# Optimization experiments

Hardware: AMD Instinct MI355X
Metric: run time of the kernel (lower is better)

## Reference

```python
import jax, jax.numpy as jnp
import numpy as np


def setup_inputs() -> dict:
    key = jax.random.key(0)
    k1, k2 = jax.random.split(key)
    L, O, N, D = 512, 512, 64, 512
    x = jax.random.normal(k1, (L, N, D), dtype=jnp.float32)
    upfold = jax.random.normal(k2, (O, N, D), dtype=jnp.float32)
    return {"x": x, "upfold": upfold}


def reference(x, upfold):
    # x: [L, N, D], upfold: [O, N, D]
    D = x.shape[-1]
    scale = 1.0 / jnp.sqrt(jnp.asarray(D, dtype=x.dtype))
    # affinities: [L, O, N]
    affinities = jnp.einsum('lnd,ond->lon', x, upfold) * scale
    # sigmoid-attention (no softmax normalization), centered at 0
    weights = jax.nn.sigmoid(affinities) - 0.5
    # features: [L, N, D]
    features = jnp.einsum('lon,ond->lnd', weights, upfold)
    return features
```

## Files before the change

### kernel.cpp

```cpp
#include <hip/hip_runtime.h>
#include <hip/hip_bf16.h>
#include <stdint.h>


typedef __attribute__((ext_vector_type(8))) short short8;
typedef __attribute__((ext_vector_type(4))) float f32x4;

__device__ __forceinline__ uint16_t f2bf(float f) {
    uint32_t u = __builtin_bit_cast(uint32_t, f);
    uint32_t r = u + 0x7FFFu + ((u >> 16) & 1u);
    return (uint16_t)(r >> 16);
}
__device__ __forceinline__ uint32_t cvt2(float a, float b) {
    return (uint32_t)f2bf(a) | ((uint32_t)f2bf(b) << 16);
}

__global__ __launch_bounds__(256) void kPrepUp(const float* __restrict__ up,
                                               uint16_t* __restrict__ ub,
                                               uint16_t* __restrict__ ut) {
    __shared__ float tile[64][65];
    int wgid = blockIdx.x;
    int iq = wgid >> 3;
    int n  = (wgid & 7) * 8 + (iq >> 6);
    int r  = iq & 63;
    int o0 = (r >> 3) << 6, d0 = (r & 7) << 6;
    int tid = threadIdx.x;
    int i  = tid >> 2;
    int jq = (tid & 3) << 4;

    const float* src = up + ((size_t)(o0 + i) * 64 + n) * 512 + d0 + jq;
    float v[16];
    #pragma unroll
    for (int c = 0; c < 16; c += 4) {
        float4 q = *reinterpret_cast<const float4*>(src + c);
        v[c] = q.x; v[c+1] = q.y; v[c+2] = q.z; v[c+3] = q.w;
        tile[i][jq+c] = q.x; tile[i][jq+c+1] = q.y;
        tile[i][jq+c+2] = q.z; tile[i][jq+c+3] = q.w;
    }
    uint32_t pk[8];
    if (ub) {
        #pragma unroll
        for (int c = 0; c < 8; ++c) pk[c] = cvt2(v[2*c], v[2*c+1]);
        uint16_t* udst = ub + ((size_t)n * 512 + o0 + i) * 512 + d0 + jq;
        *reinterpret_cast<uint4*>(udst)     = *reinterpret_cast<const uint4*>(pk);
        *reinterpret_cast<uint4*>(udst + 8) = *reinterpret_cast<const uint4*>(pk + 4);
    }
    __syncthreads();
    #pragma unroll
    for (int c = 0; c < 8; ++c) pk[c] = cvt2(tile[jq + 2*c][i], tile[jq + 2*c + 1][i]);
    uint16_t* tdst = ut + ((size_t)n * 512 + d0 + i) * 512 + o0 + jq;
    *reinterpret_cast<uint4*>(tdst)     = *reinterpret_cast<const uint4*>(pk);
    *reinterpret_cast<uint4*>(tdst + 8) = *reinterpret_cast<const uint4*>(pk + 4);
}

__global__ __launch_bounds__(256) void kPrepX(const float* __restrict__ x,
                                              uint16_t* __restrict__ xb) {
    int b = blockIdx.x;
    int tid = threadIdx.x;
    int row = b * 4 + (tid >> 6);
    int l = row >> 6, n = row & 63;
    int d0 = (tid & 63) * 8;
    const float* src = x + (size_t)row * 512 + d0;
    float4 v0 = *reinterpret_cast<const float4*>(src);
    float4 v1 = *reinterpret_cast<const float4*>(src + 4);
    uint32_t pk[4] = {cvt2(v0.x, v0.y), cvt2(v0.z, v0.w),
                      cvt2(v1.x, v1.y), cvt2(v1.z, v1.w)};
    *reinterpret_cast<uint4*>(xb + ((size_t)n * 512 + l) * 512 + d0) =
        *reinterpret_cast<const uint4*>(pk);
}

template<int MODE>
__global__ __launch_bounds__(512) void kGemmP(const uint16_t* __restrict__ A,
                                              const uint16_t* __restrict__ B,
                                              void* __restrict__ outp) {
    __shared__ __align__(16) uint16_t As[4][8192];
    __shared__ __align__(16) uint16_t Bs[4][8192];
    int bid = blockIdx.x;
    int n  = (bid & 7) * 8 + (bid >> 5);
    int t  = (bid >> 3) & 3;
    int l0 = (t >> 1) << 8, c0 = (t & 1) << 8;
    int tid = threadIdx.x, lane = tid & 63, wid = tid >> 6;
    int wr = wid >> 2, wc = wid & 3;

    const char* An = (const char*)(A + (size_t)n * 262144);
    const char* Bn = (const char*)(B + (size_t)n * 262144);

    int s1 = tid, s2 = tid + 512;
    int r1 = s1 >> 2, r2 = s2 >> 2;
    int cg1 = (s1 & 3) ^ ((r1 >> 1) & 3);
    int cg2 = (s2 & 3) ^ ((r2 >> 1) & 3);
    const char* gA1 = An + (size_t)(l0 + r1) * 1024 + cg1 * 16;
    const char* gA2 = An + (size_t)(l0 + r2) * 1024 + cg2 * 16;
    const char* gB1 = Bn + (size_t)(c0 + r1) * 1024 + cg1 * 16;
    const char* gB2 = Bn + (size_t)(c0 + r2) * 1024 + cg2 * 16;

    f32x4 acc[8][4];
    #pragma unroll
    for (int m = 0; m < 8; ++m)
        #pragma unroll
        for (int nf = 0; nf < 4; ++nf) acc[m][nf] = (f32x4)(0.f);

    auto STAGE = [&](int buf, int kt) {
        int ko = kt * 64;
        uint16_t* lA = &As[buf][wid * 512];
        uint16_t* lB = &Bs[buf][wid * 512];
        __builtin_amdgcn_global_load_lds(
            (const __attribute__((address_space(1))) uint32_t*)(gA1 + ko),
            (__attribute__((address_space(3))) uint32_t*)(lA), 16, 0, 0);
        __builtin_amdgcn_global_load_lds(
            (const __attribute__((address_space(1))) uint32_t*)(gA2 + ko),
            (__attribute__((address_space(3))) uint32_t*)(lA + 4096), 16, 0, 0);
        __builtin_amdgcn_global_load_lds(
            (const __attribute__((address_space(1))) uint32_t*)(gB1 + ko),
            (__attribute__((address_space(3))) uint32_t*)(lB), 16, 0, 0);
        __builtin_amdgcn_global_load_lds(
            (const __attribute__((address_space(1))) uint32_t*)(gB2 + ko),
            (__attribute__((address_space(3))) uint32_t*)(lB + 4096), 16, 0, 0);
    };

    STAGE(0, 0);
    STAGE(1, 1);
    STAGE(2, 2);
    asm volatile("s_waitcnt vmcnt(8)" ::: "memory");
    __builtin_amdgcn_s_barrier();
    __builtin_amdgcn_sched_barrier(0);

    int g = lane >> 4;
    #pragma unroll
    for (int kt = 0; kt < 16; ++kt) {
        const int cur = kt & 3;
        if (kt < 13) STAGE((kt + 3) & 3, kt + 3);
        const char* Ac = (const char*)As[cur];
        const char* Bc = (const char*)Bs[cur];
        short8 a[8], bb[4];
        #pragma unroll
        for (int nf = 0; nf < 4; ++nf) {
            int row = wc * 64 + nf * 16 + (lane & 15);
            int off = row * 64 + ((g ^ ((row >> 1) & 3)) << 4);
            bb[nf] = *reinterpret_cast<const short8*>(Bc + off);
        }
        #pragma unroll
        for (int m = 0; m < 8; ++m) {
            int row = wr * 128 + m * 16 + (lane & 15);
            int off = row * 64 + ((g ^ ((row >> 1) & 3)) << 4);
            a[m] = *reinterpret_cast<const short8*>(Ac + off);
        }
        __builtin_amdgcn_s_setprio(1);
        #pragma unroll
        for (int m = 0; m < 8; ++m)
            #pragma unroll
            for (int nf = 0; nf < 4; ++nf)
                acc[m][nf] = __builtin_amdgcn_mfma_f32_16x16x32_bf16(
                    a[m], bb[nf], acc[m][nf], 0, 0, 0);
        __builtin_amdgcn_s_setprio(0);
        if (kt < 13) {
            asm volatile("s_waitcnt vmcnt(8)" ::: "memory");
            __builtin_amdgcn_s_barrier();
            __builtin_amdgcn_sched_barrier(0);
        } else if (kt == 13) {
            asm volatile("s_waitcnt vmcnt(4)" ::: "memory");
            __builtin_amdgcn_s_barrier();
            __builtin_amdgcn_sched_barrier(0);
        } else if (kt == 14) {
            asm volatile("s_waitcnt vmcnt(0)" ::: "memory");
            __builtin_amdgcn_s_barrier();
            __builtin_amdgcn_sched_barrier(0);
        }
    }

    if constexpr (MODE == 1) {
        uint16_t* Wn = (uint16_t*)outp + (size_t)n * 262144;
        const float scale = 0.044194173824159216f;
        #pragma unroll
        for (int m = 0; m < 8; ++m) {
            int lrow0 = l0 + wr * 128 + m * 16 + ((lane >> 4) << 2);
            #pragma unroll
            for (int nf = 0; nf < 4; ++nf) {
                int ocol = c0 + wc * 64 + nf * 16 + (lane & 15);
                #pragma unroll
                for (int r = 0; r < 4; ++r) {
                    float aff = acc[m][nf][r] * scale;
                    float w = 1.f / (1.f + __expf(-aff)) - 0.5f;
                    Wn[(size_t)(lrow0 + r) * 512 + ocol] = f2bf(w);
                }
            }
        }
    } else {
        float* On = (float*)outp;
        #pragma unroll
        for (int m = 0; m < 8; ++m) {
            int lrow0 = l0 + wr * 128 + m * 16 + ((lane >> 4) << 2);
            #pragma unroll
            for (int nf = 0; nf < 4; ++nf) {
                int dcol = c0 + wc * 64 + nf * 16 + (lane & 15);
                #pragma unroll
                for (int r = 0; r < 4; ++r)
                    On[((size_t)(lrow0 + r) * 64 + n) * 512 + dcol] = acc[m][nf][r];
            }
        }
    }
}

__global__ __launch_bounds__(256) void kGemm1f32(const float* __restrict__ x,
                                                 const float* __restrict__ up,
                                                 uint16_t* __restrict__ W) {
    __shared__ uint16_t As[128 * 64];
    __shared__ uint16_t Bs[128 * 64];
    int b   = blockIdx.x;
    int n   = b >> 4;
    int t   = b & 15;
    int l0  = (t >> 2) << 7, o0 = (t & 3) << 7;
    int tid = threadIdx.x, lane = tid & 63, wid = tid >> 6;
    int wr = wid >> 1, wc = wid & 1;

    f32x4 acc[4][4];
    #pragma unroll
    for (int m = 0; m < 4; ++m)
        #pragma unroll
        for (int nf = 0; nf < 4; ++nf) acc[m][nf] = (f32x4)(0.f);

    int srow = tid >> 1;
    int kh   = (tid & 1) * 32;
    int swz  = (srow & 7) << 4;
    const float* aSrc = x  + ((size_t)(l0 + srow) * 64 + n) * 512 + kh;
    const float* bSrc = up + ((size_t)(o0 + srow) * 64 + n) * 512 + kh;

    for (int kt = 0; kt < 8; ++kt) {
        __syncthreads();
        const float* pA = aSrc + kt * 64;
        const float* pB = bSrc + kt * 64;
        #pragma unroll
        for (int c2 = 0; c2 < 4; ++c2) {
            float4 a0 = *reinterpret_cast<const float4*>(pA + c2 * 8);
            float4 a1 = *reinterpret_cast<const float4*>(pA + c2 * 8 + 4);
            float4 b0 = *reinterpret_cast<const float4*>(pB + c2 * 8);
            float4 b1 = *reinterpret_cast<const float4*>(pB + c2 * 8 + 4);
            uint32_t pa[4] = {cvt2(a0.x,a0.y), cvt2(a0.z,a0.w), cvt2(a1.x,a1.y), cvt2(a1.z,a1.w)};
            uint32_t pb[4] = {cvt2(b0.x,b0.y), cvt2(b0.z,b0.w), cvt2(b1.x,b1.y), cvt2(b1.z,b1.w)};
            int off = srow * 128 + (((kh * 2) + c2 * 16) ^ swz);
            *reinterpret_cast<uint4*>((char*)As + off) = *reinterpret_cast<const uint4*>(pa);
            *reinterpret_cast<uint4*>((char*)Bs + off) = *reinterpret_cast<const uint4*>(pb);
        }
        __syncthreads();
        #pragma unroll
        for (int kk = 0; kk < 2; ++kk) {
            short8 a[4], bf[4];
            int kbyte = kk * 64 + ((lane >> 4) * 16);
            #pragma unroll
            for (int m = 0; m < 4; ++m) {
                int row = wr * 64 + m * 16 + (lane & 15);
                int off = row * 128 + (kbyte ^ ((row & 7) << 4));
                a[m] = *reinterpret_cast<const short8*>((char*)As + off);
            }
            #pragma unroll
            for (int nf = 0; nf < 4; ++nf) {
                int row = wc * 64 + nf * 16 + (lane & 15);
                int off = row * 128 + (kbyte ^ ((row & 7) << 4));
                bf[nf] = *reinterpret_cast<const short8*>((char*)Bs + off);
            }
            #pragma unroll
            for (int m = 0; m < 4; ++m)
                #pragma unroll
                for (int nf = 0; nf < 4; ++nf)
                    acc[m][nf] = __builtin_amdgcn_mfma_f32_16x16x32_bf16(
                        a[m], bf[nf], acc[m][nf], 0, 0, 0);
        }
    }
    const float scale = 0.044194173824159216f;
    #pragma unroll
    for (int m = 0; m < 4; ++m) {
        int lrow0 = l0 + wr * 64 + m * 16 + ((lane >> 4) << 2);
        #pragma unroll
        for (int nf = 0; nf < 4; ++nf) {
            int ocol = o0 + wc * 64 + nf * 16 + (lane & 15);
            #pragma unroll
            for (int r = 0; r < 4; ++r) {
                float aff = acc[m][nf][r] * scale;
                float w = 1.f / (1.f + __expf(-aff)) - 0.5f;
                W[((size_t)n * 512 + (lrow0 + r)) * 512 + ocol] = f2bf(w);
            }
        }
    }
}

__global__ __launch_bounds__(256) void kGemm2Mid(const uint16_t* __restrict__ W,
                                                 const uint16_t* __restrict__ ut,
                                                 float* __restrict__ out) {
    __shared__ uint16_t As[8192];
    __shared__ uint16_t Bs[8192];
    int d = blockIdx.x;
    int n  = (d & 7) * 8 + (d >> 7);
    int t  = (d >> 3) & 15;
    int l0 = (t >> 2) << 7, c0 = (t & 3) << 7;
    int tid = threadIdx.x, lane = tid & 63, wid = tid >> 6;
    int wr = wid >> 1, wc = wid & 1;

    const char* An = (const char*)(W  + (size_t)n * 262144);
    const char* Bn = (const char*)(ut + (size_t)n * 262144);
    int rsub  = lane >> 3;
    int sbyte = ((lane & 7) ^ rsub) << 4;
    const char* gA = An + (size_t)(l0 + wid * 32 + rsub) * 1024 + sbyte;
    const char* gB = Bn + (size_t)(c0 + wid * 32 + rsub) * 1024 + sbyte;
    uint16_t* lA = As + wid * 2048;
    uint16_t* lB = Bs + wid * 2048;

    f32x4 acc[4][4];
    #pragma unroll
    for (int m = 0; m < 4; ++m)
        #pragma unroll
        for (int nf = 0; nf < 4; ++nf) acc[m][nf] = (f32x4)(0.f);

    for (int kt = 0; kt < 8; ++kt) {
        if (kt) __syncthreads();
        #pragma unroll
        for (int j = 0; j < 4; ++j) {
            __builtin_amdgcn_global_load_lds(
                (const __attribute__((address_space(1))) uint32_t*)(gA + kt * 128 + j * 8192),
                (__attribute__((address_space(3))) uint32_t*)(lA + j * 512), 16, 0, 0);
            __builtin_amdgcn_global_load_lds(
                (const __attribute__((address_space(1))) uint32_t*)(gB + kt * 128 + j * 8192),
                (__attribute__((address_space(3))) uint32_t*)(lB + j * 512), 16, 0, 0);
        }
        __syncthreads();
        #pragma unroll
        for (int kk = 0; kk < 2; ++kk) {
            short8 a[4], bb[4];
            int kbyte = kk * 64 + ((lane >> 4) * 16);
            #pragma unroll
            for (int m = 0; m < 4; ++m) {
                int row = wr * 64 + m * 16 + (lane & 15);
                int off = row * 128 + (kbyte ^ ((row & 7) << 4));
                a[m] = *reinterpret_cast<const short8*>((const char*)As + off);
            }
            #pragma unroll
            for (int nf = 0; nf < 4; ++nf) {
                int row = wc * 64 + nf * 16 + (lane & 15);
                int off = row * 128 + (kbyte ^ ((row & 7) << 4));
                bb[nf] = *reinterpret_cast<const short8*>((const char*)Bs + off);
            }
            #pragma unroll
            for (int m = 0; m < 4; ++m)
                #pragma unroll
                for (int nf = 0; nf < 4; ++nf)
                    acc[m][nf] = __builtin_amdgcn_mfma_f32_16x16x32_bf16(
                        a[m], bb[nf], acc[m][nf], 0, 0, 0);
        }
    }
    #pragma unroll
    for (int m = 0; m < 4; ++m) {
        int lrow0 = l0 + wr * 64 + m * 16 + ((lane >> 4) << 2);
        #pragma unroll
        for (int nf = 0; nf < 4; ++nf) {
            int dcol = c0 + wc * 64 + nf * 16 + (lane & 15);
            #pragma unroll
            for (int r = 0; r < 4; ++r)
                out[((size_t)(lrow0 + r) * 64 + n) * 512 + dcol] = acc[m][nf][r];
        }
    }
}

__global__ __launch_bounds__(256) void kNaive(const float* __restrict__ x,
                                              const float* __restrict__ up,
                                              float* __restrict__ out) {
    __shared__ float xr[512];
    __shared__ float w[512];
    int b = blockIdx.x;
    int l = b >> 6, n = b & 63;
    int tid = threadIdx.x;
    const float* xrow = x + ((size_t)l * 64 + n) * 512;
    xr[tid] = xrow[tid];
    xr[tid + 256] = xrow[tid + 256];
    __syncthreads();
    const float scale = 0.044194173824159216f;
    #pragma unroll
    for (int oo = 0; oo < 2; ++oo) {
        int o = tid + oo * 256;
        const float* ur = up + ((size_t)o * 64 + n) * 512;
        float s = 0.f;
        for (int dd = 0; dd < 512; ++dd) s += xr[dd] * ur[dd];
        w[o] = 1.f / (1.f + __expf(-s * scale)) - 0.5f;
    }
    __syncthreads();
    #pragma unroll
    for (int dd = 0; dd < 2; ++dd) {
        int d = tid + dd * 256;
        float f = 0.f;
        for (int o = 0; o < 512; ++o)
            f += w[o] * up[((size_t)o * 64 + n) * 512 + d];
        out[((size_t)l * 64 + n) * 512 + d] = f;
    }
}

extern "C" void kernel_launch(void* const* d_in, const int* in_sizes, int n_in,
                              void* d_out, int out_size, void* d_ws, size_t ws_size,
                              hipStream_t stream) {
    const float* x  = (const float*)d_in[0];
    const float* up = (const float*)d_in[1];
    float* out = (float*)d_out;

    const size_t MB32 = (size_t)64 * 512 * 512 * 2;
    if (ws_size >= 4 * MB32) {
        uint16_t* XB = (uint16_t*)d_ws;
        uint16_t* UB = XB + 16777216;
        uint16_t* UT = UB + 16777216;
        uint16_t* W  = UT + 16777216;
        kPrepUp<<<4096, 256, 0, stream>>>(up, UB, UT);
        kPrepX <<<8192, 256, 0, stream>>>(x, XB);
        kGemmP<1><<<256, 512, 0, stream>>>(XB, UB, W);
        kGemmP<2><<<256, 512, 0, stream>>>(W, UT, out);
    } else if (ws_size >= 2 * MB32) {
        uint16_t* UT = (uint16_t*)d_ws;
        uint16_t* W  = UT + 16777216;
        kPrepUp<<<4096, 256, 0, stream>>>(up, nullptr, UT);
        kGemm1f32<<<1024, 256, 0, stream>>>(x, up, W);
        kGemm2Mid<<<1024, 256, 0, stream>>>(W, UT, out);
    } else {
        kNaive<<<512 * 64, 256, 0, stream>>>(x, up, out);
    }
}
```

Measured before the change: 110.3 us.

## Fuse x bf16 conversion into first GEMM and split upfold prep into convert+transpose

Removes the separate x-to-bf16 prep kernel by having the first GEMM load fp32 x rows into registers, convert them with packed bf16 instructions, and write them swizzled into LDS. The loads are software-pipelined alongside async global-to-LDS loads of B. Upfold prep is split into a plain convert kernel and a bf16 LDS transpose kernel that reads the converted copy, so the transpose moves half the bytes. The change drops one 32 MB intermediate and its round trip and lowers the workspace requirement, at the cost of extra register pressure and more complex waitcnt scheduling in the GEMM.

After: 110.9 us. Within noise of the previous version (+0.5%).

```diff
diff --git a/kernel.cpp b/kernel.cpp
--- a/kernel.cpp
+++ b/kernel.cpp
@@ -14,59 +14,206 @@
 __device__ __forceinline__ uint32_t cvt2(float a, float b) {
     return (uint32_t)f2bf(a) | ((uint32_t)f2bf(b) << 16);
 }
-
-__global__ __launch_bounds__(256) void kPrepUp(const float* __restrict__ up,
-                                               uint16_t* __restrict__ ub,
-                                               uint16_t* __restrict__ ut) {
-    __shared__ float tile[64][65];
-    int wgid = blockIdx.x;
-    int iq = wgid >> 3;
-    int n  = (wgid & 7) * 8 + (iq >> 6);
-    int r  = iq & 63;
-    int o0 = (r >> 3) << 6, d0 = (r & 7) << 6;
-    int tid = threadIdx.x;
-    int i  = tid >> 2;
-    int jq = (tid & 3) << 4;
-
-    const float* src = up + ((size_t)(o0 + i) * 64 + n) * 512 + d0 + jq;
-    float v[16];
-    #pragma unroll
-    for (int c = 0; c < 16; c += 4) {
-        float4 q = *reinterpret_cast<const float4*>(src + c);
-        v[c] = q.x; v[c+1] = q.y; v[c+2] = q.z; v[c+3] = q.w;
-        tile[i][jq+c] = q.x; tile[i][jq+c+1] = q.y;
-        tile[i][jq+c+2] = q.z; tile[i][jq+c+3] = q.w;
-    }
-    uint32_t pk[8];
-    if (ub) {
-        #pragma unroll
-        for (int c = 0; c < 8; ++c) pk[c] = cvt2(v[2*c], v[2*c+1]);
-        uint16_t* udst = ub + ((size_t)n * 512 + o0 + i) * 512 + d0 + jq;
-        *reinterpret_cast<uint4*>(udst)     = *reinterpret_cast<const uint4*>(pk);
-        *reinterpret_cast<uint4*>(udst + 8) = *reinterpret_cast<const uint4*>(pk + 4);
-    }
-    __syncthreads();
-    #pragma unroll
-    for (int c = 0; c < 8; ++c) pk[c] = cvt2(tile[jq + 2*c][i], tile[jq + 2*c + 1][i]);
-    uint16_t* tdst = ut + ((size_t)n * 512 + d0 + i) * 512 + o0 + jq;
-    *reinterpret_cast<uint4*>(tdst)     = *reinterpret_cast<const uint4*>(pk);
-    *reinterpret_cast<uint4*>(tdst + 8) = *reinterpret_cast<const uint4*>(pk + 4);
-}
-
-__global__ __launch_bounds__(256) void kPrepX(const float* __restrict__ x,
-                                              uint16_t* __restrict__ xb) {
-    int b = blockIdx.x;
-    int tid = threadIdx.x;
-    int row = b * 4 + (tid >> 6);
-    int l = row >> 6, n = row & 63;
-    int d0 = (tid & 63) * 8;
-    const float* src = x + (size_t)row * 512 + d0;
+__device__ __forceinline__ uint32_t pkbf(float lo, float hi) {
+    uint32_t r;
+    asm("v_cvt_pk_bf16_f32 %0, %1, %2" : "=v"(r) : "v"(lo), "v"(hi));
+    return r;
+}
+
+__global__ __launch_bounds__(256) void kPrepU(const float* __restrict__ up,
+                                              uint16_t* __restrict__ ub) {
+    int blk  = blockIdx.x;
+    int rest = blk >> 3;
+    int n    = (blk & 7) * 8 + (rest >> 7);
+    int o    = (rest & 127) * 4 + (threadIdx.x >> 6);
+    int d0   = (threadIdx.x & 63) * 8;
+    const float* src = up + ((size_t)o * 64 + n) * 512 + d0;
     float4 v0 = *reinterpret_cast<const float4*>(src);
     float4 v1 = *reinterpret_cast<const float4*>(src + 4);
     uint32_t pk[4] = {cvt2(v0.x, v0.y), cvt2(v0.z, v0.w),
                       cvt2(v1.x, v1.y), cvt2(v1.z, v1.w)};
-    *reinterpret_cast<uint4*>(xb + ((size_t)n * 512 + l) * 512 + d0) =
+    *reinterpret_cast<uint4*>(ub + ((size_t)n * 512 + o) * 512 + d0) =
         *reinterpret_cast<const uint4*>(pk);
+}
+
+__global__ __launch_bounds__(256) void kPrepT(const uint16_t* __restrict__ ub,
+                                              uint16_t* __restrict__ ut) {
+    __shared__ uint32_t tl[512 * 20];
+    int blk  = blockIdx.x;
+    int rest = blk >> 3;
+    int n    = (blk & 7) * 8 + (rest >> 4);
+    int d0   = (rest & 15) * 32;
+    int tid  = threadIdx.x;
+
+    #pragma unroll
+    for (int e = 0; e < 2; ++e) {
+        int o = tid * 2 + e;
+        const uint16_t* src = ub + ((size_t)n * 512 + o) * 512 + d0;
+        uint4 q0 = reinterpret_cast<const uint4*>(src)[0];
+        uint4 q1 = reinterpret_cast<const uint4*>(src)[1];
+        uint4 q2 = reinterpret_cast<const uint4*>(src)[2];
+        uint4 q3 = reinterpret_cast<const uint4*>(src)[3];
+        int sw = ((o >> 6) & 3) << 2;
+        uint32_t* row = tl + o * 20;
+        *reinterpret_cast<uint4*>(row + (0  ^ sw)) = q0;
+        *reinterpret_cast<uint4*>(row + (4  ^ sw)) = q1;
+        *reinterpret_cast<uint4*>(row + (8  ^ sw)) = q2;
+        *reinterpret_cast<uint4*>(row + (12 ^ sw)) = q3;
+    }
+    __syncthreads();
+
+    int d   = tid >> 3;
+    int seg = (tid & 7) * 64;
+    int c   = d >> 1;
+    int sh  = (d & 1) * 16;
+    uint32_t ow[32];
+    #pragma unroll
+    for (int j = 0; j < 32; ++j) {
+        int o0 = seg + 2 * j;
+        int sw = ((o0 >> 6) & 3) << 2;
+        uint32_t w0 = tl[o0 * 20 + (c ^ sw)];
+        uint32_t w1 = tl[(o0 + 1) * 20 + (c ^ sw)];
+        ow[j] = ((w0 >> sh) & 0xFFFFu) | (((w1 >> sh) & 0xFFFFu) << 16);
+    }
+    uint16_t* dst = ut + ((size_t)n * 512 + d0 + d) * 512 + seg;
+    #pragma unroll
+    for (int q = 0; q < 8; ++q)
+        reinterpret_cast<uint4*>(dst)[q] = *reinterpret_cast<const uint4*>(ow + q * 4);
+}
+
+__global__ __launch_bounds__(512, 1) void kGemmP1x(const float* __restrict__ x,
+                                                   const uint16_t* __restrict__ ub,
+                                                   uint16_t* __restrict__ W) {
+    __shared__ __align__(16) uint16_t As[4][8192];
+    __shared__ __align__(16) uint16_t Bs[4][8192];
+    int bid = blockIdx.x;
+    int n  = (bid & 7) * 8 + (bid >> 5);
+    int t  = (bid >> 3) & 3;
+    int l0 = (t >> 1) << 8, c0 = (t & 1) << 8;
+    int tid = threadIdx.x, lane = tid & 63, wid = tid >> 6;
+    int wr = wid >> 2, wc = wid & 3;
+
+    const char* Bn = (const char*)(ub + (size_t)n * 262144);
+    int s1 = tid, s2 = tid + 512;
+    int r1b = s1 >> 2, r2b = s2 >> 2;
+    int cg1 = (s1 & 3) ^ ((r1b >> 1) & 3);
+    int cg2 = (s2 & 3) ^ ((r2b >> 1) & 3);
+    const char* gB1 = Bn + (size_t)(c0 + r1b) * 1024 + cg1 * 16;
+    const char* gB2 = Bn + (size_t)(c0 + r2b) * 1024 + cg2 * 16;
+
+    int ra  = tid >> 1;
+    int h   = tid & 1;
+    int swA = (ra >> 1) & 3;
+    const float* xA = x + ((size_t)(l0 + ra) * 64 + n) * 512 + h * 16;
+    int offA0 = ra * 64 + (((2 * h)     ^ swA) << 4);
+    int offA1 = ra * 64 + (((2 * h + 1) ^ swA) << 4);
+
+    f32x4 acc[8][4];
+    #pragma unroll
+    for (int m = 0; m < 8; ++m)
+        #pragma unroll
+        for (int nf = 0; nf < 4; ++nf) acc[m][nf] = (f32x4)(0.f);
+
+    auto STAGEB = [&](int buf, int kt) {
+        int ko = kt * 64;
+        uint16_t* lB = &Bs[buf][wid * 512];
+        __builtin_amdgcn_global_load_lds(
+            (const __attribute__((address_space(1))) uint32_t*)(gB1 + ko),
+            (__attribute__((address_space(3))) uint32_t*)(lB), 16, 0, 0);
+        __builtin_amdgcn_global_load_lds(
+            (const __attribute__((address_space(1))) uint32_t*)(gB2 + ko),
+            (__attribute__((address_space(3))) uint32_t*)(lB + 4096), 16, 0, 0);
+    };
+    float4 rg[2][4];
+    auto LOADR = [&](int set, int kt) {
+        const float* p = xA + kt * 32;
+        #pragma unroll
+        for (int j = 0; j < 4; ++j)
+            rg[set][j] = *reinterpret_cast<const float4*>(p + j * 4);
+    };
+    auto CVTW = [&](int set, int abuf) {
+        uint32_t pk[8];
+        #pragma unroll
+        for (int j = 0; j < 4; ++j) {
+            pk[2*j]   = pkbf(rg[set][j].x, rg[set][j].y);
+            pk[2*j+1] = pkbf(rg[set][j].z, rg[set][j].w);
+        }
+        char* base = (char*)As[abuf];
+        *reinterpret_cast<uint4*>(base + offA0) = *reinterpret_cast<const uint4*>(pk);
+        *reinterpret_cast<uint4*>(base + offA1) = *reinterpret_cast<const uint4*>(pk + 4);
+    };
+
+    LOADR(0, 0); CVTW(0, 0);
+    LOADR(0, 1); CVTW(0, 1);
+    LOADR(0, 2);
+    STAGEB(0, 0); STAGEB(1, 1); STAGEB(2, 2);
+    asm volatile("s_waitcnt vmcnt(4) lgkmcnt(0)" ::: "memory");
+    __builtin_amdgcn_s_barrier();
+    __builtin_amdgcn_sched_barrier(0);
+
+    int g = lane >> 4;
+    #pragma unroll
+    for (int kt = 0; kt < 16; ++kt) {
+        const int cur = kt & 3;
+        if (kt < 13) {
+            LOADR((kt + 1) & 1, kt + 3);
+            STAGEB((kt + 3) & 3, kt + 3);
+        }
+        const char* Ac = (const char*)As[cur];
+        const char* Bc = (const char*)Bs[cur];
+        short8 a[8], bb[4];
+        #pragma unroll
+        for (int nf = 0; nf < 4; ++nf) {
+            int row = wc * 64 + nf * 16 + (lane & 15);
+            int off = row * 64 + ((g ^ ((row >> 1) & 3)) << 4);
+            bb[nf] = *reinterpret_cast<const short8*>(Bc + off);
+        }
+        #pragma unroll
+        for (int m = 0; m < 8; ++m) {
+            int row = wr * 128 + m * 16 + (lane & 15);
+            int off = row * 64 + ((g ^ ((row >> 1) & 3)) << 4);
+            a[m] = *reinterpret_cast<const short8*>(Ac + off);
+        }
+        __builtin_amdgcn_s_setprio(1);
+        #pragma unroll
+        for (int m = 0; m < 8; ++m)
+            #pragma unroll
+            for (int nf = 0; nf < 4; ++nf)
+                acc[m][nf] = __builtin_amdgcn_mfma_f32_16x16x32_bf16(
+                    a[m], bb[nf], acc[m][nf], 0, 0, 0);
+        __builtin_amdgcn_s_setprio(0);
+        if (kt < 14) CVTW(kt & 1, (kt + 2) & 3);
+        if (kt < 13) {
+            asm volatile("s_waitcnt vmcnt(8) lgkmcnt(0)" ::: "memory");
+            __builtin_amdgcn_s_barrier();
+            __builtin_amdgcn_sched_barrier(0);
+        } else if (kt == 13) {
+            asm volatile("s_waitcnt vmcnt(2) lgkmcnt(0)" ::: "memory");
+            __builtin_amdgcn_s_barrier();
+            __builtin_amdgcn_sched_barrier(0);
+        } else if (kt == 14) {
+            asm volatile("s_waitcnt vmcnt(0) lgkmcnt(0)" ::: "memory");
+            __builtin_amdgcn_s_barrier();
+            __builtin_amdgcn_sched_barrier(0);
+        }
+    }
+
+    uint16_t* Wn = W + (size_t)n * 262144;
+    const float scale = 0.044194173824159216f;
+    #pragma unroll
+    for (int m = 0; m < 8; ++m) {
+        int lrow0 = l0 + wr * 128 + m * 16 + ((lane >> 4) << 2);
+        #pragma unroll
+        for (int nf = 0; nf < 4; ++nf) {
+            int ocol = c0 + wc * 64 + nf * 16 + (lane & 15);
+            #pragma unroll
+            for (int r = 0; r < 4; ++r) {
+                float aff = acc[m][nf][r] * scale;
+                float w = 1.f / (1.f + __expf(-aff)) - 0.5f;
+                Wn[(size_t)(lrow0 + r) * 512 + ocol] = f2bf(w);
+            }
+        }
+    }
 }
 
 template<int MODE>
@@ -84,7 +231,6 @@
 
     const char* An = (const char*)(A + (size_t)n * 262144);
     const char* Bn = (const char*)(B + (size_t)n * 262144);
-
     int s1 = tid, s2 = tid + 512;
     int r1 = s1 >> 2, r2 = s2 >> 2;
     int cg1 = (s1 & 3) ^ ((r1 >> 1) & 3);
@@ -201,6 +347,44 @@
     }
 }
 
+__global__ __launch_bounds__(256) void kPrepUp(const float* __restrict__ up,
+                                               uint16_t* __restrict__ ub,
+                                               uint16_t* __restrict__ ut) {
+    __shared__ float tile[64][65];
+    int wgid = blockIdx.x;
+    int iq = wgid >> 3;
+    int n  = (wgid & 7) * 8 + (iq >> 6);
+    int r  = iq & 63;
+    int o0 = (r >> 3) << 6, d0 = (r & 7) << 6;
+    int tid = threadIdx.x;
+    int i  = tid >> 2;
+    int jq = (tid & 3) << 4;
+
+    const float* src = up + ((size_t)(o0 + i) * 64 + n) * 512 + d0 + jq;
+    float v[16];
+    #pragma unroll
+    for (int c = 0; c < 16; c += 4) {
+        float4 q = *reinterpret_cast<const float4*>(src + c);
+        v[c] = q.x; v[c+1] = q.y; v[c+2] = q.z; v[c+3] = q.w;
+        tile[i][jq+c] = q.x; tile[i][jq+c+1] = q.y;
+        tile[i][jq+c+2] = q.z; tile[i][jq+c+3] = q.w;
+    }
+    uint32_t pk[8];
+    if (ub) {
+        #pragma unroll
+        for (int c = 0; c < 8; ++c) pk[c] = cvt2(v[2*c], v[2*c+1]);
+        uint16_t* udst = ub + ((size_t)n * 512 + o0 + i) * 512 + d0 + jq;
+        *reinterpret_cast<uint4*>(udst)     = *reinterpret_cast<const uint4*>(pk);
+        *reinterpret_cast<uint4*>(udst + 8) = *reinterpret_cast<const uint4*>(pk + 4);
+    }
+    __syncthreads();
+    #pragma unroll
+    for (int c = 0; c < 8; ++c) pk[c] = cvt2(tile[jq + 2*c][i], tile[jq + 2*c + 1][i]);
+    uint16_t* tdst = ut + ((size_t)n * 512 + d0 + i) * 512 + o0 + jq;
+    *reinterpret_cast<uint4*>(tdst)     = *reinterpret_cast<const uint4*>(pk);
+    *reinterpret_cast<uint4*>(tdst + 8) = *reinterpret_cast<const uint4*>(pk + 4);
+}
+
 __global__ __launch_bounds__(256) void kGemm1f32(const float* __restrict__ x,
                                                  const float* __restrict__ up,
                                                  uint16_t* __restrict__ W) {
@@ -399,14 +583,13 @@
     float* out = (float*)d_out;
 
     const size_t MB32 = (size_t)64 * 512 * 512 * 2;
-    if (ws_size >= 4 * MB32) {
-        uint16_t* XB = (uint16_t*)d_ws;
-        uint16_t* UB = XB + 16777216;
+    if (ws_size >= 3 * MB32) {
+        uint16_t* UB = (uint16_t*)d_ws;
         uint16_t* UT = UB + 16777216;
         uint16_t* W  = UT + 16777216;
-        kPrepUp<<<4096, 256, 0, stream>>>(up, UB, UT);
-        kPrepX <<<8192, 256, 0, stream>>>(x, XB);
-        kGemmP<1><<<256, 512, 0, stream>>>(XB, UB, W);
+        kPrepU<<<8192, 256, 0, stream>>>(up, UB);
+        kPrepT<<<1024, 256, 0, stream>>>(UB, UT);
+        kGemmP1x<<<256, 512, 0, stream>>>(x, UB, W);
         kGemmP<2><<<256, 512, 0, stream>>>(W, UT, out);
     } else if (ws_size >= 2 * MB32) {
         uint16_t* UT = (uint16_t*)d_ws;
```

## Split upfold prep into row-wise bf16 cast and separate bf16 transpose kernel

Applied to the files above, without the earlier changes.

Replaces the combined fp32 tile-transpose prep with a simple coalesced fp32-to-bf16 cast kernel, followed by a new kernel that transposes the already-converted bf16 buffer through a swizzled LDS tile. The aim is fully coalesced row-wise fp32 reads and a transpose that moves half as many bytes. The cost is an extra launch and re-reading the bf16 copy of upfold. The s_setprio hints around the MFMA loop in the GEMM are also removed.

Result: slower. 117.9 us (+6.9%).

```diff
diff --git a/kernel.cpp b/kernel.cpp
--- a/kernel.cpp
+++ b/kernel.cpp
@@ -15,42 +15,20 @@
     return (uint32_t)f2bf(a) | ((uint32_t)f2bf(b) << 16);
 }
 
-__global__ __launch_bounds__(256) void kPrepUp(const float* __restrict__ up,
-                                               uint16_t* __restrict__ ub,
-                                               uint16_t* __restrict__ ut) {
-    __shared__ float tile[64][65];
-    int wgid = blockIdx.x;
-    int iq = wgid >> 3;
-    int n  = (wgid & 7) * 8 + (iq >> 6);
-    int r  = iq & 63;
-    int o0 = (r >> 3) << 6, d0 = (r & 7) << 6;
-    int tid = threadIdx.x;
-    int i  = tid >> 2;
-    int jq = (tid & 3) << 4;
-
-    const float* src = up + ((size_t)(o0 + i) * 64 + n) * 512 + d0 + jq;
-    float v[16];
-    #pragma unroll
-    for (int c = 0; c < 16; c += 4) {
-        float4 q = *reinterpret_cast<const float4*>(src + c);
-        v[c] = q.x; v[c+1] = q.y; v[c+2] = q.z; v[c+3] = q.w;
-        tile[i][jq+c] = q.x; tile[i][jq+c+1] = q.y;
-        tile[i][jq+c+2] = q.z; tile[i][jq+c+3] = q.w;
-    }
-    uint32_t pk[8];
-    if (ub) {
-        #pragma unroll
-        for (int c = 0; c < 8; ++c) pk[c] = cvt2(v[2*c], v[2*c+1]);
-        uint16_t* udst = ub + ((size_t)n * 512 + o0 + i) * 512 + d0 + jq;
-        *reinterpret_cast<uint4*>(udst)     = *reinterpret_cast<const uint4*>(pk);
-        *reinterpret_cast<uint4*>(udst + 8) = *reinterpret_cast<const uint4*>(pk + 4);
-    }
-    __syncthreads();
-    #pragma unroll
-    for (int c = 0; c < 8; ++c) pk[c] = cvt2(tile[jq + 2*c][i], tile[jq + 2*c + 1][i]);
-    uint16_t* tdst = ut + ((size_t)n * 512 + d0 + i) * 512 + o0 + jq;
-    *reinterpret_cast<uint4*>(tdst)     = *reinterpret_cast<const uint4*>(pk);
-    *reinterpret_cast<uint4*>(tdst + 8) = *reinterpret_cast<const uint4*>(pk + 4);
+__global__ __launch_bounds__(256) void kPrepU(const float* __restrict__ up,
+                                              uint16_t* __restrict__ ub) {
+    int blk  = blockIdx.x;
+    int rest = blk >> 3;
+    int n    = (blk & 7) * 8 + (rest >> 7);
+    int o    = (rest & 127) * 4 + (threadIdx.x >> 6);
+    int d0   = (threadIdx.x & 63) * 8;
+    const float* src = up + ((size_t)o * 64 + n) * 512 + d0;
+    float4 v0 = *reinterpret_cast<const float4*>(src);
+    float4 v1 = *reinterpret_cast<const float4*>(src + 4);
+    uint32_t pk[4] = {cvt2(v0.x, v0.y), cvt2(v0.z, v0.w),
+                      cvt2(v1.x, v1.y), cvt2(v1.z, v1.w)};
+    *reinterpret_cast<uint4*>(ub + ((size_t)n * 512 + o) * 512 + d0) =
+        *reinterpret_cast<const uint4*>(pk);
 }
 
 __global__ __launch_bounds__(256) void kPrepX(const float* __restrict__ x,
@@ -67,6 +45,51 @@
                       cvt2(v1.x, v1.y), cvt2(v1.z, v1.w)};
     *reinterpret_cast<uint4*>(xb + ((size_t)n * 512 + l) * 512 + d0) =
         *reinterpret_cast<const uint4*>(pk);
+}
+
+__global__ __launch_bounds__(256) void kPrepT(const uint16_t* __restrict__ ub,
+                                              uint16_t* __restrict__ ut) {
+    __shared__ uint32_t tl[512 * 20];
+    int blk  = blockIdx.x;
+    int rest = blk >> 3;
+    int n    = (blk & 7) * 8 + (rest >> 4);
+    int d0   = (rest & 15) * 32;
+    int tid  = threadIdx.x;
+
+    #pragma unroll
+    for (int e = 0; e < 2; ++e) {
+        int o = tid * 2 + e;
+        const uint16_t* src = ub + ((size_t)n * 512 + o) * 512 + d0;
+        uint4 q0 = reinterpret_cast<const uint4*>(src)[0];
+        uint4 q1 = reinterpret_cast<const uint4*>(src)[1];
+        uint4 q2 = reinterpret_cast<const uint4*>(src)[2];
+        uint4 q3 = reinterpret_cast<const uint4*>(src)[3];
+        int sw = ((o >> 6) & 3) << 2;
+        uint32_t* row = tl + o * 20;
+        *reinterpret_cast<uint4*>(row + (0  ^ sw)) = q0;
+        *reinterpret_cast<uint4*>(row + (4  ^ sw)) = q1;
+        *reinterpret_cast<uint4*>(row + (8  ^ sw)) = q2;
+        *reinterpret_cast<uint4*>(row + (12 ^ sw)) = q3;
+    }
+    __syncthreads();
+
+    int d   = tid >> 3;
+    int seg = (tid & 7) * 64;
+    int c   = d >> 1;
+    int sh  = (d & 1) * 16;
+    uint32_t ow[32];
+    #pragma unroll
+    for (int j = 0; j < 32; ++j) {
+        int o0 = seg + 2 * j;
+        int sw = ((o0 >> 6) & 3) << 2;
+        uint32_t w0 = tl[o0 * 20 + (c ^ sw)];
+        uint32_t w1 = tl[(o0 + 1) * 20 + (c ^ sw)];
+        ow[j] = ((w0 >> sh) & 0xFFFFu) | (((w1 >> sh) & 0xFFFFu) << 16);
+    }
+    uint16_t* dst = ut + ((size_t)n * 512 + d0 + d) * 512 + seg;
+    #pragma unroll
+    for (int q = 0; q < 8; ++q)
+        reinterpret_cast<uint4*>(dst)[q] = *reinterpret_cast<const uint4*>(ow + q * 4);
 }
 
 template<int MODE>
@@ -145,14 +168,12 @@
             int off = row * 64 + ((g ^ ((row >> 1) & 3)) << 4);
             a[m] = *reinterpret_cast<const short8*>(Ac + off);
         }
-        __builtin_amdgcn_s_setprio(1);
         #pragma unroll
         for (int m = 0; m < 8; ++m)
             #pragma unroll
             for (int nf = 0; nf < 4; ++nf)
                 acc[m][nf] = __builtin_amdgcn_mfma_f32_16x16x32_bf16(
                     a[m], bb[nf], acc[m][nf], 0, 0, 0);
-        __builtin_amdgcn_s_setprio(0);
         if (kt < 13) {
             asm volatile("s_waitcnt vmcnt(8)" ::: "memory");
             __builtin_amdgcn_s_barrier();
@@ -199,6 +220,44 @@
             }
         }
     }
+}
+
+__global__ __launch_bounds__(256) void kPrepUp(const float* __restrict__ up,
+                                               uint16_t* __restrict__ ub,
+                                               uint16_t* __restrict__ ut) {
+    __shared__ float tile[64][65];
+    int wgid = blockIdx.x;
+    int iq = wgid >> 3;
+    int n  = (wgid & 7) * 8 + (iq >> 6);
+    int r  = iq & 63;
+    int o0 = (r >> 3) << 6, d0 = (r & 7) << 6;
+    int tid = threadIdx.x;
+    int i  = tid >> 2;
+    int jq = (tid & 3) << 4;
+
+    const float* src = up + ((size_t)(o0 + i) * 64 + n) * 512 + d0 + jq;
+    float v[16];
+    #pragma unroll
+    for (int c = 0; c < 16; c += 4) {
+        float4 q = *reinterpret_cast<const float4*>(src + c);
+        v[c] = q.x; v[c+1] = q.y; v[c+2] = q.z; v[c+3] = q.w;
+        tile[i][jq+c] = q.x; tile[i][jq+c+1] = q.y;
+        tile[i][jq+c+2] = q.z; tile[i][jq+c+3] = q.w;
+    }
+    uint32_t pk[8];
+    if (ub) {
+        #pragma unroll
+        for (int c = 0; c < 8; ++c) pk[c] = cvt2(v[2*c], v[2*c+1]);
+        uint16_t* udst = ub + ((size_t)n * 512 + o0 + i) * 512 + d0 + jq;
+        *reinterpret_cast<uint4*>(udst)     = *reinterpret_cast<const uint4*>(pk);
+        *reinterpret_cast<uint4*>(udst + 8) = *reinterpret_cast<const uint4*>(pk + 4);
+    }
+    __syncthreads();
+    #pragma unroll
+    for (int c = 0; c < 8; ++c) pk[c] = cvt2(tile[jq + 2*c][i], tile[jq + 2*c + 1][i]);
+    uint16_t* tdst = ut + ((size_t)n * 512 + d0 + i) * 512 + o0 + jq;
+    *reinterpret_cast<uint4*>(tdst)     = *reinterpret_cast<const uint4*>(pk);
+    *reinterpret_cast<uint4*>(tdst + 8) = *reinterpret_cast<const uint4*>(pk + 4);
 }
 
 __global__ __launch_bounds__(256) void kGemm1f32(const float* __restrict__ x,
@@ -404,8 +463,9 @@
         uint16_t* UB = XB + 16777216;
         uint16_t* UT = UB + 16777216;
         uint16_t* W  = UT + 16777216;
-        kPrepUp<<<4096, 256, 0, stream>>>(up, UB, UT);
-        kPrepX <<<8192, 256, 0, stream>>>(x, XB);
+        kPrepU<<<8192, 256, 0, stream>>>(up, UB);
+        kPrepX<<<8192, 256, 0, stream>>>(x, XB);
+        kPrepT<<<1024, 256, 0, stream>>>(UB, UT);
         kGemmP<1><<<256, 512, 0, stream>>>(XB, UB, W);
         kGemmP<2><<<256, 512, 0, stream>>>(W, UT, out);
     } else if (ws_size >= 2 * MB32) {
```
